# Optimization experiments

Measured on AMD Instinct MI355X. Metric: run time of the kernel, lower is better.

Reference implementation:

```python
import jax, jax.numpy as jnp
import numpy as np

B, T, N_EMBD, H = 8, 2048, 1024, 128

def setup_inputs() -> dict:
    key = jax.random.key(0)
    k1, k2, k3, k4 = jax.random.split(key, 4)
    x = jax.random.normal(k1, (B, T, N_EMBD), dtype=jnp.float32)
    s = 1.0 / np.sqrt(N_EMBD).astype(np.float32)
    Wq = jax.random.normal(k2, (N_EMBD, H), dtype=jnp.float32) * s
    Wk = jax.random.normal(k3, (N_EMBD, H), dtype=jnp.float32) * s
    Wv = jax.random.normal(k4, (N_EMBD, H), dtype=jnp.float32) * s
    return {"x": x, "Wq": Wq, "Wk": Wk, "Wv": Wv}

def reference(x, Wq, Wk, Wv):
    # x: [B,T,C]; projections (no bias per init_kwargs)
    q = x @ Wq  # [B,T,H]
    k = x @ Wk  # [B,T,H]
    v = x @ Wv  # [B,T,H]
    scale = jnp.asarray(k.shape[-1], x.dtype) ** -0.5
    att = jnp.einsum('bth,bsh->bts', q, k) * scale  # [B,T,T]
    Tlen = x.shape[1]
    causal = jnp.tril(jnp.ones((Tlen, Tlen), dtype=bool))  # bias buffer tril mask
    att = jnp.where(causal, att, jnp.asarray(-jnp.inf, att.dtype))
    att = jax.nn.softmax(att, axis=-1)
    # dropout omitted (eval mode / deterministic reference)
    y = jnp.einsum('bts,bsh->bth', att, v)  # [B,T,H]
    return y
```

## Files before the change

### kernel.cpp

```cpp
#include <hip/hip_runtime.h>
#include <hip/hip_bf16.h>
#include <stdint.h>

#define BB 8
#define TT 2048
#define CC 1024
#define HH 128
#define VTP 2112

typedef __attribute__((ext_vector_type(8))) short bf16x8;
typedef __attribute__((ext_vector_type(8))) unsigned short u16x8;
typedef __attribute__((ext_vector_type(4))) float f32x4;
typedef __attribute__((ext_vector_type(8))) _Float16 h16x8;

static __device__ __forceinline__ unsigned short f2bf(float f) {
    union { float f; uint32_t u; } v; v.f = f;
    return (unsigned short)((v.u + 0x7fffu + ((v.u >> 16) & 1u)) >> 16);
}

#define GLOBAL_AS __attribute__((address_space(1)))
#define LDS_AS    __attribute__((address_space(3)))
static __device__ __forceinline__ void async16(const void* g, void* l) {
    __builtin_amdgcn_global_load_lds((const GLOBAL_AS void*)g, (LDS_AS void*)l, 16, 0, 0);
}

__global__ __launch_bounds__(256) void wconv(
    const float* __restrict__ Wq, const float* __restrict__ Wk,
    const float* __restrict__ Wv, unsigned short* __restrict__ Wb)
{
    int u = blockIdx.x * 256 + threadIdx.x;
    if (u >= 3 * 128 * 128) return;
    int kc = u & 127, n = (u >> 7) & 127, mat = u >> 14;
    const float* W = (mat == 0) ? Wq : (mat == 1) ? Wk : Wv;
    const float* s = W + (size_t)(kc * 8) * HH + n;
    u16x8 v;
    #pragma unroll
    for (int j = 0; j < 8; j++) v[j] = f2bf(s[(size_t)j * HH]);
    *(u16x8*)(Wb + ((size_t)mat * HH + n) * CC + kc * 8) = v;
}

#define BS_U16 4608
#define EQ_OFF 0
#define EK_OFF 8704
#define EV_OFF 17408
__global__ __launch_bounds__(512) void qkv_proj(
    const float* __restrict__ x, const unsigned short* __restrict__ Wb,
    unsigned short* __restrict__ Q, unsigned short* __restrict__ K,
    unsigned short* __restrict__ Vt)
{
    __shared__ __align__(16) unsigned short lds[29184];

    const int m0  = blockIdx.x * 64;
    const int tid = threadIdx.x;
    const int lane = tid & 63;
    const int w    = tid >> 6;
    const int qd   = lane >> 4;
    const int ln   = lane & 15;
    const int wm   = w & 1;
    const int wn   = w >> 1;

    f32x4 acc[2][6];
    #pragma unroll
    for (int i = 0; i < 2; i++)
        #pragma unroll
        for (int j = 0; j < 6; j++) acc[i][j] = (f32x4){0.f,0.f,0.f,0.f};

    const int xr = tid >> 3;
    const int xg = (tid & 7) * 8;

    float4 xf[2];
    {
        const float* s = x + (size_t)(m0 + xr) * CC + xg;
        xf[0] = ((const float4*)s)[0];
        xf[1] = ((const float4*)s)[1];
    }

    for (int k0 = 0; k0 < CC; k0 += 64) {
        {
            u16x8 v0;
            v0[0]=f2bf(xf[0].x); v0[1]=f2bf(xf[0].y); v0[2]=f2bf(xf[0].z); v0[3]=f2bf(xf[0].w);
            v0[4]=f2bf(xf[1].x); v0[5]=f2bf(xf[1].y); v0[6]=f2bf(xf[1].z); v0[7]=f2bf(xf[1].w);
            *(u16x8*)&lds[xr * 72 + xg] = v0;
        }
        #pragma unroll
        for (int i = 0; i < 6; i++) {
            int sb = i * 512 + w * 64;
            int slot = sb + lane;
            int row = slot >> 3, j = (slot & 7) ^ (row & 7);
            async16(Wb + (size_t)row * CC + k0 + j * 8, &lds[BS_U16 + sb * 8]);
        }
        __syncthreads();
        if (k0 + 64 < CC) {
            const float* s = x + (size_t)(m0 + xr) * CC + k0 + 64 + xg;
            xf[0] = ((const float4*)s)[0];
            xf[1] = ((const float4*)s)[1];
        }
        #pragma unroll
        for (int ks = 0; ks < 2; ks++) {
            bf16x8 a0 = *(const bf16x8*)&lds[(wm*32 + ln) * 72 + ks*32 + qd*8];
            bf16x8 a1 = *(const bf16x8*)&lds[(wm*32 + 16 + ln) * 72 + ks*32 + qd*8];
            #pragma unroll
            for (int nf = 0; nf < 6; nf++) {
                int row = wn * 96 + nf * 16 + ln;
                int ch  = (ks * 4 + qd) ^ (row & 7);
                bf16x8 b = *(const bf16x8*)&lds[BS_U16 + (row * 8 + ch) * 8];
                acc[0][nf] = __builtin_amdgcn_mfma_f32_16x16x32_bf16(a0, b, acc[0][nf], 0, 0, 0);
                acc[1][nf] = __builtin_amdgcn_mfma_f32_16x16x32_bf16(a1, b, acc[1][nf], 0, 0, 0);
            }
        }
        __syncthreads();
    }

    #pragma unroll
    for (int mf = 0; mf < 2; mf++)
        #pragma unroll
        for (int nf = 0; nf < 6; nf++) {
            int n = wn * 96 + nf * 16;
            int mat = n >> 7, hb = n & 127;
            #pragma unroll
            for (int r = 0; r < 4; r++) {
                unsigned short v = f2bf(acc[mf][nf][r]);
                int mrow = wm*32 + mf*16 + qd*4 + r;
                if (mat < 2) lds[(mat ? EK_OFF : EQ_OFF) + mrow * 136 + hb + ln] = v;
                else         lds[EV_OFF + (hb + ln) * 72 + mrow] = v;
            }
        }
    __syncthreads();
    {
        int rr = tid >> 3, c0 = (tid & 7) * 16;
        #pragma unroll
        for (int i = 0; i < 2; i++) {
            u16x8 vq = *(const u16x8*)&lds[EQ_OFF + rr * 136 + c0 + i * 8];
            *(u16x8*)(Q + (size_t)(m0 + rr) * HH + c0 + i * 8) = vq;
            u16x8 vk = *(const u16x8*)&lds[EK_OFF + rr * 136 + c0 + i * 8];
            *(u16x8*)(K + (size_t)(m0 + rr) * HH + c0 + i * 8) = vk;
        }
    }
    {
        int bb = m0 >> 11, t0 = m0 & (TT - 1);
        int hh = tid >> 2, tf = (tid & 3) * 16;
        #pragma unroll
        for (int i = 0; i < 2; i++) {
            u16x8 vv = *(const u16x8*)&lds[EV_OFF + hh * 72 + tf + i * 8];
            *(u16x8*)(Vt + ((size_t)bb * HH + hh) * VTP + t0 + tf + i * 8) = vv;
        }
    }
}

__global__ __launch_bounds__(512) void attn(
    const unsigned short* __restrict__ Q, const unsigned short* __restrict__ K,
    const unsigned short* __restrict__ Vt, float* __restrict__ out)
{
    __shared__ __align__(16) _Float16 Om[8][16 * 128];
    __shared__ __align__(16) unsigned short Ps[8][16 * 40];
    __shared__ float Lp[8][16];

    const int tid  = threadIdx.x;
    const int lane = tid & 63;
    const int wave = tid >> 6;
    const int qd = lane >> 4;
    const int ln = lane & 15;
    const int qgrp = wave >> 2;
    const int kq4  = wave & 3;

    const int bx = blockIdx.x;
    int b, qt;
    if (bx < 256) { b = bx & 7;               qt = 63 - (bx >> 3); }
    else          { int u = bx - 256; b = u & 7; qt = u >> 3; }
    const int qbase = qt * 32 + qgrp * 16;
    const int nst = (qt + 4) >> 2;

    const unsigned short* Qb = Q  + (size_t)b * TT * HH;
    const unsigned short* Kb = K  + (size_t)b * TT * HH;
    const unsigned short* Vb = Vt + (size_t)b * HH * VTP;

    bf16x8 aq[4];
    #pragma unroll
    for (int c = 0; c < 4; c++)
        aq[c] = *(const bf16x8*)(Qb + (size_t)(qbase + ln) * HH + c * 32 + qd * 8);

    f32x4 O[8];
    float lsum[4];
    #pragma unroll
    for (int h = 0; h < 8; h++) O[h] = (f32x4){0.f,0.f,0.f,0.f};
    #pragma unroll
    for (int r = 0; r < 4; r++) lsum[r] = 0.f;

    const float sl   = 0.08838834764831843f * 1.4426950408889634f;
    const float M0L2 = 7.2134752044448f;
    unsigned short* ps = Ps[wave];

    for (int st = 0; st < nst; st++) {
        const int s0 = st * 128;

        f32x4 s[2] = {(f32x4){0.f,0.f,0.f,0.f}, (f32x4){0.f,0.f,0.f,0.f}};
        #pragma unroll
        for (int nt = 0; nt < 2; nt++) {
            const unsigned short* kr = Kb + (size_t)(s0 + kq4*32 + nt*16 + ln) * HH;
            #pragma unroll
            for (int c = 0; c < 4; c++) {
                bf16x8 bk = *(const bf16x8*)(kr + (c*4 + qd) * 8);
                s[nt] = __builtin_amdgcn_mfma_f32_16x16x32_bf16(aq[c], bk, s[nt], 0, 0, 0);
            }
        }
        #pragma unroll
        for (int nt = 0; nt < 2; nt++) {
            int col = s0 + kq4 * 32 + nt * 16 + ln;
            #pragma unroll
            for (int r = 0; r < 4; r++) {
                int row = qbase + qd * 4 + r;
                float e = __builtin_amdgcn_exp2f(s[nt][r] * sl - M0L2);
                e = (col <= row) ? e : 0.f;
                lsum[r] += e;
                ps[(qd*4 + r) * 40 + nt*16 + ln] = f2bf(e);
            }
        }
        bf16x8 ap = *(const bf16x8*)&ps[ln * 40 + qd * 8];
        #pragma unroll
        for (int ht = 0; ht < 8; ht++) {
            bf16x8 bv = *(const bf16x8*)(Vb + (size_t)(ht*16 + ln) * VTP + s0 + kq4*32 + qd*8);
            O[ht] = __builtin_amdgcn_mfma_f32_16x16x32_bf16(ap, bv, O[ht], 0, 0, 0);
        }
    }

    #pragma unroll
    for (int r = 0; r < 4; r++) {
        float sum = lsum[r];
        #pragma unroll
        for (int off = 1; off < 16; off <<= 1)
            sum += __shfl_xor(sum, off, 64);
        if (ln == 0) Lp[wave][qd*4 + r] = sum;
    }
    _Float16* om = &Om[wave][0];
    #pragma unroll
    for (int ht = 0; ht < 8; ht++)
        #pragma unroll
        for (int r = 0; r < 4; r++)
            om[(qd*4 + r) * 128 + ht*16 + ln] = (_Float16)O[ht][r];
    __syncthreads();

    {
        int row = tid >> 4, h0 = (tid & 15) * 8;
        int g = row >> 4, q = row & 15;
        float L = Lp[g*4 + 0][q] + Lp[g*4 + 1][q] + Lp[g*4 + 2][q] + Lp[g*4 + 3][q];
        float inv = 1.0f / L;
        const _Float16* p0 = &Om[g*4 + 0][q * 128 + h0];
        const _Float16* p1 = &Om[g*4 + 1][q * 128 + h0];
        const _Float16* p2 = &Om[g*4 + 2][q * 128 + h0];
        const _Float16* p3 = &Om[g*4 + 3][q * 128 + h0];
        float* op = out + ((size_t)b * TT + qt * 32 + row) * HH + h0;
        #pragma unroll
        for (int i = 0; i < 2; i++) {
            float4 v;
            v.x = (((float)p0[i*4+0] + (float)p1[i*4+0]) + ((float)p2[i*4+0] + (float)p3[i*4+0])) * inv;
            v.y = (((float)p0[i*4+1] + (float)p1[i*4+1]) + ((float)p2[i*4+1] + (float)p3[i*4+1])) * inv;
            v.z = (((float)p0[i*4+2] + (float)p1[i*4+2]) + ((float)p2[i*4+2] + (float)p3[i*4+2])) * inv;
            v.w = (((float)p0[i*4+3] + (float)p1[i*4+3]) + ((float)p2[i*4+3] + (float)p3[i*4+3])) * inv;
            ((float4*)op)[i] = v;
        }
    }
}

extern "C" void kernel_launch(void* const* d_in, const int* in_sizes, int n_in,
                              void* d_out, int out_size, void* d_ws, size_t ws_size,
                              hipStream_t stream) {
    const float* x  = (const float*)d_in[0];
    const float* Wq = (const float*)d_in[1];
    const float* Wk = (const float*)d_in[2];
    const float* Wv = (const float*)d_in[3];

    unsigned short* Wb = (unsigned short*)d_ws;
    unsigned short* Qw = Wb + (size_t)3 * HH * CC;
    unsigned short* Kw = Qw + (size_t)BB * TT * HH;
    unsigned short* Vw = Kw + (size_t)BB * TT * HH;

    wconv<<<dim3(192), 256, 0, stream>>>(Wq, Wk, Wv, Wb);
    qkv_proj<<<dim3(256), 512, 0, stream>>>(x, Wb, Qw, Kw, Vw);
    attn<<<dim3(512), 512, 0, stream>>>(Qw, Kw, Vw, (float*)d_out);
}
```

Measured before the change: 180.3 us.

## Stage K/V tiles in LDS with async double-buffering and 64-row query blocks

The attention kernel now uses 1024-thread blocks that each cover 64 query rows. Per 128-key step, K and V^T tiles are copied into swizzled LDS with async global-to-LDS loads and double buffering, so all 16 waves share one tile instead of each wave reading global memory on its own. The epilogue reuses the K buffer for partial outputs, and the grid shrinks to 256 blocks with about 149 KB of dynamic LDS. This cuts redundant global/L2 traffic but adds a block-wide barrier on every step and gives only one block per CU, which lowers occupancy. The heavy-tile-first ordering of blocks is also dropped.

New measurement: 148.8 us. 17.5% less time.

```diff
diff --git a/kernel.cpp b/kernel.cpp
--- a/kernel.cpp
+++ b/kernel.cpp
@@ -147,13 +147,15 @@
     }
 }
 
-__global__ __launch_bounds__(512) void attn(
+__global__ __launch_bounds__(1024) void attn(
     const unsigned short* __restrict__ Q, const unsigned short* __restrict__ K,
     const unsigned short* __restrict__ Vt, float* __restrict__ out)
 {
-    __shared__ __align__(16) _Float16 Om[8][16 * 128];
-    __shared__ __align__(16) unsigned short Ps[8][16 * 40];
-    __shared__ float Lp[8][16];
+    extern __shared__ __align__(16) unsigned short dyn[];
+    unsigned short* KsB = dyn;
+    unsigned short* VsB = dyn + 32768;
+    unsigned short* PsB = dyn + 65536;
+    float*          Lp  = (float*)(dyn + 75776);
 
     const int tid  = threadIdx.x;
     const int lane = tid & 63;
@@ -161,14 +163,13 @@
     const int qd = lane >> 4;
     const int ln = lane & 15;
     const int qgrp = wave >> 2;
-    const int kq4  = wave & 3;
+    const int kq   = wave & 3;
 
     const int bx = blockIdx.x;
-    int b, qt;
-    if (bx < 256) { b = bx & 7;               qt = 63 - (bx >> 3); }
-    else          { int u = bx - 256; b = u & 7; qt = u >> 3; }
-    const int qbase = qt * 32 + qgrp * 16;
-    const int nst = (qt + 4) >> 2;
+    const int b  = bx & 7;
+    const int qt = bx >> 3;
+    const int qbase = qt * 64 + qgrp * 16;
+    const int nst = (qt + 2) >> 1;
 
     const unsigned short* Qb = Q  + (size_t)b * TT * HH;
     const unsigned short* Kb = K  + (size_t)b * TT * HH;
@@ -188,24 +189,50 @@
 
     const float sl   = 0.08838834764831843f * 1.4426950408889634f;
     const float M0L2 = 7.2134752044448f;
-    unsigned short* ps = Ps[wave];
-
+    unsigned short* ps = PsB + wave * 640;
+
+    #define STAGE(S0, BUF)                                                              \
+        do {                                                                            \
+            _Pragma("unroll")                                                           \
+            for (int i = 0; i < 2; i++) {                                               \
+                int sb = i * 1024 + wave * 64;                                          \
+                int slot = sb + lane;                                                   \
+                int row = slot >> 4, jj = (slot & 15) ^ (row & 15);                     \
+                async16(Kb + (size_t)((S0) + row) * HH + jj * 8,                        \
+                        KsB + (size_t)(BUF) * 16384 + sb * 8);                          \
+            }                                                                           \
+            _Pragma("unroll")                                                           \
+            for (int i = 0; i < 2; i++) {                                               \
+                int sb = i * 1024 + wave * 64;                                          \
+                int slot = sb + lane;                                                   \
+                int row = slot >> 4, jj = (slot & 15) ^ (row & 15);                     \
+                async16(Vb + (size_t)row * VTP + (S0) + jj * 8,                         \
+                        VsB + (size_t)(BUF) * 16384 + sb * 8);                          \
+            }                                                                           \
+        } while (0)
+
+    STAGE(0, 0);
     for (int st = 0; st < nst; st++) {
+        __syncthreads();
+        if (st + 1 < nst) STAGE((st + 1) * 128, (st + 1) & 1);
+        const int buf = st & 1;
+        const unsigned short* Ks = KsB + (size_t)buf * 16384;
+        const unsigned short* Vs = VsB + (size_t)buf * 16384;
         const int s0 = st * 128;
 
         f32x4 s[2] = {(f32x4){0.f,0.f,0.f,0.f}, (f32x4){0.f,0.f,0.f,0.f}};
         #pragma unroll
         for (int nt = 0; nt < 2; nt++) {
-            const unsigned short* kr = Kb + (size_t)(s0 + kq4*32 + nt*16 + ln) * HH;
+            int krow = kq * 32 + nt * 16;
             #pragma unroll
             for (int c = 0; c < 4; c++) {
-                bf16x8 bk = *(const bf16x8*)(kr + (c*4 + qd) * 8);
+                bf16x8 bk = *(const bf16x8*)&Ks[(krow + ln) * 128 + (((c*4 + qd) ^ ln)) * 8];
                 s[nt] = __builtin_amdgcn_mfma_f32_16x16x32_bf16(aq[c], bk, s[nt], 0, 0, 0);
             }
         }
         #pragma unroll
         for (int nt = 0; nt < 2; nt++) {
-            int col = s0 + kq4 * 32 + nt * 16 + ln;
+            int col = s0 + kq * 32 + nt * 16 + ln;
             #pragma unroll
             for (int r = 0; r < 4; r++) {
                 int row = qbase + qd * 4 + r;
@@ -218,20 +245,22 @@
         bf16x8 ap = *(const bf16x8*)&ps[ln * 40 + qd * 8];
         #pragma unroll
         for (int ht = 0; ht < 8; ht++) {
-            bf16x8 bv = *(const bf16x8*)(Vb + (size_t)(ht*16 + ln) * VTP + s0 + kq4*32 + qd*8);
+            int vrow = ht * 16 + ln;
+            bf16x8 bv = *(const bf16x8*)&Vs[vrow * 128 + (((kq*4 + qd) ^ ln)) * 8];
             O[ht] = __builtin_amdgcn_mfma_f32_16x16x32_bf16(ap, bv, O[ht], 0, 0, 0);
         }
     }
 
+    __syncthreads();
     #pragma unroll
     for (int r = 0; r < 4; r++) {
         float sum = lsum[r];
         #pragma unroll
         for (int off = 1; off < 16; off <<= 1)
             sum += __shfl_xor(sum, off, 64);
-        if (ln == 0) Lp[wave][qd*4 + r] = sum;
-    }
-    _Float16* om = &Om[wave][0];
+        if (ln == 0) Lp[wave * 16 + qd*4 + r] = sum;
+    }
+    _Float16* om = (_Float16*)KsB + (size_t)wave * 16 * 128;
     #pragma unroll
     for (int ht = 0; ht < 8; ht++)
         #pragma unroll
@@ -242,13 +271,14 @@
     {
         int row = tid >> 4, h0 = (tid & 15) * 8;
         int g = row >> 4, q = row & 15;
-        float L = Lp[g*4 + 0][q] + Lp[g*4 + 1][q] + Lp[g*4 + 2][q] + Lp[g*4 + 3][q];
+        float L = Lp[(g*4 + 0)*16 + q] + Lp[(g*4 + 1)*16 + q]
+                + Lp[(g*4 + 2)*16 + q] + Lp[(g*4 + 3)*16 + q];
         float inv = 1.0f / L;
-        const _Float16* p0 = &Om[g*4 + 0][q * 128 + h0];
-        const _Float16* p1 = &Om[g*4 + 1][q * 128 + h0];
-        const _Float16* p2 = &Om[g*4 + 2][q * 128 + h0];
-        const _Float16* p3 = &Om[g*4 + 3][q * 128 + h0];
-        float* op = out + ((size_t)b * TT + qt * 32 + row) * HH + h0;
+        const _Float16* p0 = (const _Float16*)KsB + (size_t)(g*4 + 0) * 2048 + q * 128 + h0;
+        const _Float16* p1 = p0 + 2048;
+        const _Float16* p2 = p1 + 2048;
+        const _Float16* p3 = p2 + 2048;
+        float* op = out + ((size_t)b * TT + qt * 64 + row) * HH + h0;
         #pragma unroll
         for (int i = 0; i < 2; i++) {
             float4 v;
@@ -259,6 +289,7 @@
             ((float4*)op)[i] = v;
         }
     }
+    #undef STAGE
 }
 
 extern "C" void kernel_launch(void* const* d_in, const int* in_sizes, int n_in,
@@ -274,7 +305,14 @@
     unsigned short* Kw = Qw + (size_t)BB * TT * HH;
     unsigned short* Vw = Kw + (size_t)BB * TT * HH;
 
+    static bool attr_done = false;
+    if (!attr_done) {
+        hipFuncSetAttribute((const void*)attn,
+                            hipFuncAttributeMaxDynamicSharedMemorySize, 152576);
+        attr_done = true;
+    }
+
     wconv<<<dim3(192), 256, 0, stream>>>(Wq, Wk, Wv, Wb);
     qkv_proj<<<dim3(256), 512, 0, stream>>>(x, Wb, Qw, Kw, Vw);
-    attn<<<dim3(512), 512, 0, stream>>>(Qw, Kw, Vw, (float*)d_out);
-}
+    attn<<<dim3(256), 1024, 152576, stream>>>(Qw, Kw, Vw, (float*)d_out);
+}
```

## Store Q/K/V in MFMA fragment-major layout for contiguous attention loads

Applied to the files above, without the earlier changes.

The projection kernel now writes Q, K and V in a fragment-ordered layout, so each 64-lane MFMA operand block is a contiguous 1 KB chunk. The attention kernel then loads K and V fragments with a single lane-linear 16-byte load per lane instead of strided row loads (256-byte stride for K, padded-row stride for transposed V). This is meant to make global loads fully coalesced and reduce address arithmetic in the inner loop. The cost is more complex indexing in the projection epilogue, and the padded Vt layout is dropped.

Result: faster. 156.0 us (-13.5%).

```diff
diff --git a/kernel.cpp b/kernel.cpp
--- a/kernel.cpp
+++ b/kernel.cpp
@@ -6,12 +6,10 @@
 #define TT 2048
 #define CC 1024
 #define HH 128
-#define VTP 2112
 
 typedef __attribute__((ext_vector_type(8))) short bf16x8;
 typedef __attribute__((ext_vector_type(8))) unsigned short u16x8;
 typedef __attribute__((ext_vector_type(4))) float f32x4;
-typedef __attribute__((ext_vector_type(8))) _Float16 h16x8;
 
 static __device__ __forceinline__ unsigned short f2bf(float f) {
     union { float f; uint32_t u; } v; v.f = f;
@@ -23,6 +21,7 @@
 static __device__ __forceinline__ void async16(const void* g, void* l) {
     __builtin_amdgcn_global_load_lds((const GLOBAL_AS void*)g, (LDS_AS void*)l, 16, 0, 0);
 }
+
 
 __global__ __launch_bounds__(256) void wconv(
     const float* __restrict__ Wq, const float* __restrict__ Wk,
@@ -45,8 +44,8 @@
 #define EV_OFF 17408
 __global__ __launch_bounds__(512) void qkv_proj(
     const float* __restrict__ x, const unsigned short* __restrict__ Wb,
-    unsigned short* __restrict__ Q, unsigned short* __restrict__ K,
-    unsigned short* __restrict__ Vt)
+    unsigned short* __restrict__ QF, unsigned short* __restrict__ KF,
+    unsigned short* __restrict__ VF)
 {
     __shared__ __align__(16) unsigned short lds[29184];
 
@@ -128,12 +127,16 @@
     __syncthreads();
     {
         int rr = tid >> 3, c0 = (tid & 7) * 16;
+        int kbg = (m0 + rr) >> 4, lnr = rr & 15;
         #pragma unroll
         for (int i = 0; i < 2; i++) {
+            int c8 = (c0 >> 3) + i;
+            int db = c8 >> 2, qdw = c8 & 3;
+            size_t a = ((size_t)kbg * 4 + db) * 512 + qdw * 128 + lnr * 8;
             u16x8 vq = *(const u16x8*)&lds[EQ_OFF + rr * 136 + c0 + i * 8];
-            *(u16x8*)(Q + (size_t)(m0 + rr) * HH + c0 + i * 8) = vq;
+            *(u16x8*)(QF + a) = vq;
             u16x8 vk = *(const u16x8*)&lds[EK_OFF + rr * 136 + c0 + i * 8];
-            *(u16x8*)(K + (size_t)(m0 + rr) * HH + c0 + i * 8) = vk;
+            *(u16x8*)(KF + a) = vk;
         }
     }
     {
@@ -141,15 +144,18 @@
         int hh = tid >> 2, tf = (tid & 3) * 16;
         #pragma unroll
         for (int i = 0; i < 2; i++) {
+            int k0 = t0 + tf + i * 8;
+            size_t a = (((size_t)(bb * 64 + (k0 >> 5))) * 8 + (hh >> 4)) * 512
+                     + ((k0 >> 3) & 3) * 128 + (hh & 15) * 8;
             u16x8 vv = *(const u16x8*)&lds[EV_OFF + hh * 72 + tf + i * 8];
-            *(u16x8*)(Vt + ((size_t)bb * HH + hh) * VTP + t0 + tf + i * 8) = vv;
+            *(u16x8*)(VF + a) = vv;
         }
     }
 }
 
 __global__ __launch_bounds__(512) void attn(
-    const unsigned short* __restrict__ Q, const unsigned short* __restrict__ K,
-    const unsigned short* __restrict__ Vt, float* __restrict__ out)
+    const unsigned short* __restrict__ QF, const unsigned short* __restrict__ KF,
+    const unsigned short* __restrict__ VF, float* __restrict__ out)
 {
     __shared__ __align__(16) _Float16 Om[8][16 * 128];
     __shared__ __align__(16) unsigned short Ps[8][16 * 40];
@@ -161,23 +167,22 @@
     const int qd = lane >> 4;
     const int ln = lane & 15;
     const int qgrp = wave >> 2;
-    const int kq4  = wave & 3;
+    const int kq   = wave & 3;
 
     const int bx = blockIdx.x;
     int b, qt;
     if (bx < 256) { b = bx & 7;               qt = 63 - (bx >> 3); }
     else          { int u = bx - 256; b = u & 7; qt = u >> 3; }
-    const int qbase = qt * 32 + qgrp * 16;
+    const int qrow0 = qt * 32 + qgrp * 16;
     const int nst = (qt + 4) >> 2;
 
-    const unsigned short* Qb = Q  + (size_t)b * TT * HH;
-    const unsigned short* Kb = K  + (size_t)b * TT * HH;
-    const unsigned short* Vb = Vt + (size_t)b * HH * VTP;
-
     bf16x8 aq[4];
-    #pragma unroll
-    for (int c = 0; c < 4; c++)
-        aq[c] = *(const bf16x8*)(Qb + (size_t)(qbase + ln) * HH + c * 32 + qd * 8);
+    {
+        const unsigned short* qp = QF + ((size_t)(b * 128 + qt * 2 + qgrp) * 4) * 512 + lane * 8;
+        #pragma unroll
+        for (int c = 0; c < 4; c++)
+            aq[c] = *(const bf16x8*)(qp + c * 512);
+    }
 
     f32x4 O[8];
     float lsum[4];
@@ -190,25 +195,29 @@
     const float M0L2 = 7.2134752044448f;
     unsigned short* ps = Ps[wave];
 
+    const unsigned short* kp = KF + (size_t)(b * 128 + kq * 2) * 2048 + lane * 8;
+    const unsigned short* vp = VF + (size_t)(b * 64 + kq) * 4096 + lane * 8;
+
     for (int st = 0; st < nst; st++) {
         const int s0 = st * 128;
+        const unsigned short* kst = kp + (size_t)st * 16384;
+        const unsigned short* vst = vp + (size_t)st * 16384;
 
         f32x4 s[2] = {(f32x4){0.f,0.f,0.f,0.f}, (f32x4){0.f,0.f,0.f,0.f}};
         #pragma unroll
         for (int nt = 0; nt < 2; nt++) {
-            const unsigned short* kr = Kb + (size_t)(s0 + kq4*32 + nt*16 + ln) * HH;
             #pragma unroll
             for (int c = 0; c < 4; c++) {
-                bf16x8 bk = *(const bf16x8*)(kr + (c*4 + qd) * 8);
+                bf16x8 bk = *(const bf16x8*)(kst + nt * 2048 + c * 512);
                 s[nt] = __builtin_amdgcn_mfma_f32_16x16x32_bf16(aq[c], bk, s[nt], 0, 0, 0);
             }
         }
         #pragma unroll
         for (int nt = 0; nt < 2; nt++) {
-            int col = s0 + kq4 * 32 + nt * 16 + ln;
+            int col = s0 + kq * 32 + nt * 16 + ln;
             #pragma unroll
             for (int r = 0; r < 4; r++) {
-                int row = qbase + qd * 4 + r;
+                int row = qrow0 + qd * 4 + r;
                 float e = __builtin_amdgcn_exp2f(s[nt][r] * sl - M0L2);
                 e = (col <= row) ? e : 0.f;
                 lsum[r] += e;
@@ -218,7 +227,7 @@
         bf16x8 ap = *(const bf16x8*)&ps[ln * 40 + qd * 8];
         #pragma unroll
         for (int ht = 0; ht < 8; ht++) {
-            bf16x8 bv = *(const bf16x8*)(Vb + (size_t)(ht*16 + ln) * VTP + s0 + kq4*32 + qd*8);
+            bf16x8 bv = *(const bf16x8*)(vst + ht * 512);
             O[ht] = __builtin_amdgcn_mfma_f32_16x16x32_bf16(ap, bv, O[ht], 0, 0, 0);
         }
     }
@@ -241,13 +250,14 @@
 
     {
         int row = tid >> 4, h0 = (tid & 15) * 8;
-        int g = row >> 4, q = row & 15;
-        float L = Lp[g*4 + 0][q] + Lp[g*4 + 1][q] + Lp[g*4 + 2][q] + Lp[g*4 + 3][q];
+        int g = row >> 4, rl = row & 15;
+        float L = Lp[g*4 + 0][rl] + Lp[g*4 + 1][rl]
+                + Lp[g*4 + 2][rl] + Lp[g*4 + 3][rl];
         float inv = 1.0f / L;
-        const _Float16* p0 = &Om[g*4 + 0][q * 128 + h0];
-        const _Float16* p1 = &Om[g*4 + 1][q * 128 + h0];
-        const _Float16* p2 = &Om[g*4 + 2][q * 128 + h0];
-        const _Float16* p3 = &Om[g*4 + 3][q * 128 + h0];
+        const _Float16* p0 = &Om[g*4 + 0][rl * 128 + h0];
+        const _Float16* p1 = &Om[g*4 + 1][rl * 128 + h0];
+        const _Float16* p2 = &Om[g*4 + 2][rl * 128 + h0];
+        const _Float16* p3 = &Om[g*4 + 3][rl * 128 + h0];
         float* op = out + ((size_t)b * TT + qt * 32 + row) * HH + h0;
         #pragma unroll
         for (int i = 0; i < 2; i++) {
@@ -270,11 +280,11 @@
     const float* Wv = (const float*)d_in[3];
 
     unsigned short* Wb = (unsigned short*)d_ws;
-    unsigned short* Qw = Wb + (size_t)3 * HH * CC;
-    unsigned short* Kw = Qw + (size_t)BB * TT * HH;
-    unsigned short* Vw = Kw + (size_t)BB * TT * HH;
+    unsigned short* QFw = Wb + (size_t)3 * HH * CC;
+    unsigned short* KFw = QFw + (size_t)BB * TT * HH;
+    unsigned short* VFw = KFw + (size_t)BB * TT * HH;
 
     wconv<<<dim3(192), 256, 0, stream>>>(Wq, Wk, Wv, Wb);
-    qkv_proj<<<dim3(256), 512, 0, stream>>>(x, Wb, Qw, Kw, Vw);
-    attn<<<dim3(512), 512, 0, stream>>>(Qw, Kw, Vw, (float*)d_out);
-}
+    qkv_proj<<<dim3(256), 512, 0, stream>>>(x, Wb, QFw, KFw, VFw);
+    attn<<<dim3(512), 512, 0, stream>>>(QFw, KFw, VFw, (float*)d_out);
+}
```
